# Performance work log

Measured on AMD Instinct MI355X. Metric: run time of the kernel, lower is better.

Reference implementation:

```python
import jax, jax.numpy as jnp
import numpy as np

P, R, S = 512, 128, 128   # num_proposal, ref_length, src_length
K = 3                      # top-k per row/column
THRESHOLD = 0.05
MUTUAL = False
CONDITIONAL = True


def setup_inputs() -> dict:
    key = jax.random.key(0)
    k1, k2, k3, k4 = jax.random.split(key, 4)
    return {
        "matching_score_map": jax.random.normal(k1, (P, R, S), dtype=jnp.float32),
        "ref_knn_masks": jax.random.bernoulli(k2, 0.9, (P, R)),
        "src_knn_masks": jax.random.bernoulli(k3, 0.9, (P, S)),
        "node_corr_scores": jax.random.uniform(k4, (P,), dtype=jnp.float32),
    }


def reference(matching_score_map, ref_knn_masks, src_knn_masks, node_corr_scores):
    # matching_score_map: [P, R, S] log-scores -> exp, as in torch forward
    m = jnp.exp(matching_score_map)
    p, r, s = m.shape
    # corr_mask_map = ref_mask[:, :, None] & src_mask[:, None, :] -> [P, R, S]
    corr_mask_map = jnp.logical_and(ref_knn_masks[:, :, None], src_knn_masks[:, None, :])

    pidx = jnp.arange(p)[:, None, None]

    # top-k along src dim (dim=2), scatter back into a sparse score map
    ref_topk_scores, ref_topk_idx = jax.lax.top_k(m, K)           # [P, R, K]
    ridx = jnp.arange(r)[None, :, None]
    ref_score_map = jnp.zeros_like(m).at[pidx, ridx, ref_topk_idx].set(ref_topk_scores)

    # top-k along ref dim (dim=1): transpose, top_k, scatter, transpose back
    mt = jnp.swapaxes(m, 1, 2)                                    # [P, S, R]
    src_topk_scores, src_topk_idx = jax.lax.top_k(mt, K)          # [P, S, K]
    sidx = jnp.arange(s)[None, :, None]
    src_score_map = jnp.swapaxes(
        jnp.zeros_like(mt).at[pidx, sidx, src_topk_idx].set(src_topk_scores), 1, 2
    )

    ref_corr_map = jnp.logical_and(ref_score_map > THRESHOLD, corr_mask_map)
    src_corr_map = jnp.logical_and(src_score_map > THRESHOLD, corr_mask_map)

    score_map = (ref_score_map + src_score_map) * 0.5
    if MUTUAL:
        corr_map = jnp.logical_and(ref_corr_map, src_corr_map)
    else:
        corr_map = jnp.logical_or(ref_corr_map, src_corr_map)
    if CONDITIONAL:
        score_map = score_map * node_corr_scores[:, None, None]
    return score_map, corr_map
```

## Files before the change

### kernel.cpp

```cpp
#include <hip/hip_runtime.h>


constexpr int NP = 512;
constexpr int NR = 128;
constexpr int NS = 128;
constexpr int RS = NR * NS;
constexpr float THRESHOLD = 0.05f;
constexpr float NEG_INF = -3.4e38f;

__device__ __forceinline__ void top3_insert(float v, float& m0, float& m1, float& m2) {
    bool g2 = v > m2, g1 = v > m1, g0 = v > m0;
    float n2 = g1 ? m1 : (g2 ? v : m2);
    float n1 = g0 ? m0 : (g1 ? v : m1);
    float n0 = g0 ? v : m0;
    m0 = n0; m1 = n1; m2 = n2;
}

__device__ __forceinline__ float third_of_merge(float a0, float a1, float a2,
                                                float b0, float b1, float b2) {
    float third = NEG_INF;
    #pragma unroll
    for (int k = 0; k < 3; ++k) {
        bool ta = a0 >= b0;
        third = ta ? a0 : b0;
        float na0 = ta ? a1 : a0, na1 = ta ? a2 : a1;
        float nb0 = ta ? b0 : b1, nb1 = ta ? b1 : b2;
        a0 = na0; a1 = na1; a2 = ta ? NEG_INF : a2;
        b0 = nb0; b1 = nb1; b2 = ta ? b2 : NEG_INF;
    }
    return third;
}

__global__ __launch_bounds__(256) void thresholds_kernel(
    const float* __restrict__ in, float* __restrict__ ws)
{
    const int b = blockIdx.x;
    const int p = b >> 1;
    const int t = threadIdx.x;
    const float* base = in + (size_t)p * RS;
    __shared__ float mbuf[NS * 3];

    if (b & 1) {
        const int row = t >> 1, half = t & 1;
        const float4* r4 = (const float4*)(base + row * NS + half * 64);
        float m0 = NEG_INF, m1 = NEG_INF, m2 = NEG_INF;
        #pragma unroll
        for (int k = 0; k < 16; ++k) {
            float4 v = r4[k];
            top3_insert(v.x, m0, m1, m2);
            top3_insert(v.y, m0, m1, m2);
            top3_insert(v.z, m0, m1, m2);
            top3_insert(v.w, m0, m1, m2);
        }
        float o0 = __shfl_xor(m0, 1);
        float o1 = __shfl_xor(m1, 1);
        float o2 = __shfl_xor(m2, 1);
        float third = third_of_merge(m0, m1, m2, o0, o1, o2);
        if (half == 0) ws[p * 256 + 128 + row] = third;
    } else {
        const int col = t & 127, rh = t >> 7;
        const float* c0 = base + (size_t)(rh * 64) * NS + col;
        float m0 = NEG_INF, m1 = NEG_INF, m2 = NEG_INF;
        #pragma unroll 16
        for (int r = 0; r < 64; ++r)
            top3_insert(c0[r * NS], m0, m1, m2);
        if (rh) {
            mbuf[col * 3 + 0] = m0; mbuf[col * 3 + 1] = m1; mbuf[col * 3 + 2] = m2;
        }
        __syncthreads();
        if (!rh) {
            float third = third_of_merge(m0, m1, m2,
                                         mbuf[col * 3], mbuf[col * 3 + 1], mbuf[col * 3 + 2]);
            ws[p * 256 + col] = third;
        }
    }
}

__global__ __launch_bounds__(256) void epilogue_kernel(
    const float* __restrict__ in,
    const int*   __restrict__ rmask,
    const int*   __restrict__ smask,
    const float* __restrict__ ncs,
    const float* __restrict__ ws,
    float*       __restrict__ out)
{
    const int gid = blockIdx.x * 256 + threadIdx.x;
    const int p   = gid >> 12;
    const int rem = gid & 4095;
    const int r   = rem >> 5;
    const int c4  = rem & 31;

    const float4 x   = ((const float4*)in)[gid];
    const float  tr  = ws[p * 256 + 128 + r];
    const float4 tc  = ((const float4*)(ws + p * 256))[c4];
    const bool   mr  = rmask[p * NR + r] != 0;
    const int4   ms  = ((const int4*)(smask + (size_t)p * NS))[c4];
    const float  nc  = ncs[p];

    float4 sc, co;
    {   float m  = __expf(x.x);
        float rs = (x.x >= tr)   ? m : 0.f;
        float cs = (x.x >= tc.x) ? m : 0.f;
        sc.x = 0.5f * (rs + cs) * nc;
        co.x = (mr && (ms.x != 0) && (rs > THRESHOLD || cs > THRESHOLD)) ? 1.f : 0.f; }
    {   float m  = __expf(x.y);
        float rs = (x.y >= tr)   ? m : 0.f;
        float cs = (x.y >= tc.y) ? m : 0.f;
        sc.y = 0.5f * (rs + cs) * nc;
        co.y = (mr && (ms.y != 0) && (rs > THRESHOLD || cs > THRESHOLD)) ? 1.f : 0.f; }
    {   float m  = __expf(x.z);
        float rs = (x.z >= tr)   ? m : 0.f;
        float cs = (x.z >= tc.z) ? m : 0.f;
        sc.z = 0.5f * (rs + cs) * nc;
        co.z = (mr && (ms.z != 0) && (rs > THRESHOLD || cs > THRESHOLD)) ? 1.f : 0.f; }
    {   float m  = __expf(x.w);
        float rs = (x.w >= tr)   ? m : 0.f;
        float cs = (x.w >= tc.w) ? m : 0.f;
        sc.w = 0.5f * (rs + cs) * nc;
        co.w = (mr && (ms.w != 0) && (rs > THRESHOLD || cs > THRESHOLD)) ? 1.f : 0.f; }

    ((float4*)out)[gid] = sc;
    ((float4*)(out + (size_t)NP * RS))[gid] = co;
}

extern "C" void kernel_launch(void* const* d_in, const int* in_sizes, int n_in,
                              void* d_out, int out_size, void* d_ws, size_t ws_size,
                              hipStream_t stream) {
    const float* msm   = (const float*)d_in[0];
    const int*   rmask = (const int*)  d_in[1];
    const int*   smask = (const int*)  d_in[2];
    const float* ncs   = (const float*)d_in[3];
    float* out = (float*)d_out;
    float* ws  = (float*)d_ws;

    thresholds_kernel<<<2 * NP, 256, 0, stream>>>(msm, ws);
    epilogue_kernel<<<NP * RS / 4 / 256, 256, 0, stream>>>(msm, rmask, smask, ncs, ws, out);
}
```

Measured before the change: 110.1 us.

## Fuse top-k threshold and epilogue kernels via per-proposal LDS tile

Replaces the two-kernel design with one kernel that runs one 512-thread block per proposal. Each block stages the whole 128x128 score tile in LDS, computes the row and column third-largest thresholds with shuffle-based top-3 merges, then applies the exp/threshold/mask epilogue from LDS. This removes the second global read of the input and one kernel launch. In exchange, 64KB of LDS per block limits blocks per CU, and with only 512 blocks there is little overlap between the load, compute and store phases; the column pass may also hit LDS bank conflicts.

```diff
diff --git a/kernel.cpp b/kernel.cpp
--- a/kernel.cpp
+++ b/kernel.cpp
@@ -16,111 +16,120 @@
     m0 = n0; m1 = n1; m2 = n2;
 }
 
-__device__ __forceinline__ float third_of_merge(float a0, float a1, float a2,
-                                                float b0, float b1, float b2) {
-    float third = NEG_INF;
-    #pragma unroll
-    for (int k = 0; k < 3; ++k) {
-        bool ta = a0 >= b0;
-        third = ta ? a0 : b0;
-        float na0 = ta ? a1 : a0, na1 = ta ? a2 : a1;
-        float nb0 = ta ? b0 : b1, nb1 = ta ? b1 : b2;
-        a0 = na0; a1 = na1; a2 = ta ? NEG_INF : a2;
-        b0 = nb0; b1 = nb1; b2 = ta ? b2 : NEG_INF;
-    }
-    return third;
+__device__ __forceinline__ void shfl_merge3(int d, float& m0, float& m1, float& m2) {
+    float o0 = __shfl_xor(m0, d);
+    float o1 = __shfl_xor(m1, d);
+    float o2 = __shfl_xor(m2, d);
+    top3_insert(o0, m0, m1, m2);
+    top3_insert(o1, m0, m1, m2);
+    top3_insert(o2, m0, m1, m2);
 }
 
-__global__ __launch_bounds__(256) void thresholds_kernel(
-    const float* __restrict__ in, float* __restrict__ ws)
+__global__ __launch_bounds__(512, 4) void fused_kernel(
+    const float* __restrict__ in,
+    const int*   __restrict__ rmask,
+    const int*   __restrict__ smask,
+    const float* __restrict__ ncs,
+    float*       __restrict__ ws,
+    float*       __restrict__ out)
 {
-    const int b = blockIdx.x;
-    const int p = b >> 1;
+    __shared__ float tile[RS];
+    const int p = blockIdx.x;
     const int t = threadIdx.x;
-    const float* base = in + (size_t)p * RS;
-    __shared__ float mbuf[NS * 3];
 
-    if (b & 1) {
-        const int row = t >> 1, half = t & 1;
-        const float4* r4 = (const float4*)(base + row * NS + half * 64);
+    const float4* b4 = (const float4*)(in + (size_t)p * RS);
+    float4*       t4 = (float4*)tile;
+
+    #pragma unroll
+    for (int k = 0; k < 8; ++k) {
+        int i4 = t + k * 512;
+        t4[i4] = b4[i4];
+    }
+    __syncthreads();
+
+    float* ws_row = ws + (size_t)p * 256;
+    float* ws_col = ws_row + 128;
+
+    {
+        const int row = t >> 2, q = t & 3;
+        const int base4 = row * 32 + q * 8;
         float m0 = NEG_INF, m1 = NEG_INF, m2 = NEG_INF;
         #pragma unroll
-        for (int k = 0; k < 16; ++k) {
-            float4 v = r4[k];
+        for (int j = 0; j < 8; ++j) {
+            int jj = (j + t) & 7;
+            float4 v = t4[base4 + jj];
             top3_insert(v.x, m0, m1, m2);
             top3_insert(v.y, m0, m1, m2);
             top3_insert(v.z, m0, m1, m2);
             top3_insert(v.w, m0, m1, m2);
         }
-        float o0 = __shfl_xor(m0, 1);
-        float o1 = __shfl_xor(m1, 1);
-        float o2 = __shfl_xor(m2, 1);
-        float third = third_of_merge(m0, m1, m2, o0, o1, o2);
-        if (half == 0) ws[p * 256 + 128 + row] = third;
-    } else {
-        const int col = t & 127, rh = t >> 7;
-        const float* c0 = base + (size_t)(rh * 64) * NS + col;
+        shfl_merge3(1, m0, m1, m2);
+        shfl_merge3(2, m0, m1, m2);
+        if (q == 0) ws_row[row] = m2;
+    }
+
+    {
+        const int col = t >> 2, seg = t & 3;
         float m0 = NEG_INF, m1 = NEG_INF, m2 = NEG_INF;
-        #pragma unroll 16
-        for (int r = 0; r < 64; ++r)
-            top3_insert(c0[r * NS], m0, m1, m2);
-        if (rh) {
-            mbuf[col * 3 + 0] = m0; mbuf[col * 3 + 1] = m1; mbuf[col * 3 + 2] = m2;
+        #pragma unroll 8
+        for (int i = 0; i < 32; ++i) {
+            float v = tile[(seg * 32 + i) * NS + col];
+            top3_insert(v, m0, m1, m2);
         }
-        __syncthreads();
-        if (!rh) {
-            float third = third_of_merge(m0, m1, m2,
-                                         mbuf[col * 3], mbuf[col * 3 + 1], mbuf[col * 3 + 2]);
-            ws[p * 256 + col] = third;
-        }
+        shfl_merge3(1, m0, m1, m2);
+        shfl_merge3(2, m0, m1, m2);
+        if (seg == 0) ws_col[col] = m2;
     }
-}
 
-__global__ __launch_bounds__(256) void epilogue_kernel(
-    const float* __restrict__ in,
-    const int*   __restrict__ rmask,
-    const int*   __restrict__ smask,
-    const float* __restrict__ ncs,
-    const float* __restrict__ ws,
-    float*       __restrict__ out)
-{
-    const int gid = blockIdx.x * 256 + threadIdx.x;
-    const int p   = gid >> 12;
-    const int rem = gid & 4095;
-    const int r   = rem >> 5;
-    const int c4  = rem & 31;
+    __threadfence_block();
+    __syncthreads();
 
-    const float4 x   = ((const float4*)in)[gid];
-    const float  tr  = ws[p * 256 + 128 + r];
-    const float4 tc  = ((const float4*)(ws + p * 256))[c4];
-    const bool   mr  = rmask[p * NR + r] != 0;
-    const int4   ms  = ((const int4*)(smask + (size_t)p * NS))[c4];
-    const float  nc  = ncs[p];
+    const float  nc = ncs[p];
+    const float4 tc = ((const float4*)ws_col)[t & 31];
+    const int4   ms = ((const int4*)(smask + (size_t)p * NS))[t & 31];
+    float trow[8];
+    int   mrow[8];
+    #pragma unroll
+    for (int k = 0; k < 8; ++k) {
+        int row = (t >> 5) + k * 16;
+        trow[k] = ws_row[row];
+        mrow[k] = rmask[p * NR + row];
+    }
 
-    float4 sc, co;
-    {   float m  = __expf(x.x);
-        float rs = (x.x >= tr)   ? m : 0.f;
-        float cs = (x.x >= tc.x) ? m : 0.f;
-        sc.x = 0.5f * (rs + cs) * nc;
-        co.x = (mr && (ms.x != 0) && (rs > THRESHOLD || cs > THRESHOLD)) ? 1.f : 0.f; }
-    {   float m  = __expf(x.y);
-        float rs = (x.y >= tr)   ? m : 0.f;
-        float cs = (x.y >= tc.y) ? m : 0.f;
-        sc.y = 0.5f * (rs + cs) * nc;
-        co.y = (mr && (ms.y != 0) && (rs > THRESHOLD || cs > THRESHOLD)) ? 1.f : 0.f; }
-    {   float m  = __expf(x.z);
-        float rs = (x.z >= tr)   ? m : 0.f;
-        float cs = (x.z >= tc.z) ? m : 0.f;
-        sc.z = 0.5f * (rs + cs) * nc;
-        co.z = (mr && (ms.z != 0) && (rs > THRESHOLD || cs > THRESHOLD)) ? 1.f : 0.f; }
-    {   float m  = __expf(x.w);
-        float rs = (x.w >= tr)   ? m : 0.f;
-        float cs = (x.w >= tc.w) ? m : 0.f;
-        sc.w = 0.5f * (rs + cs) * nc;
-        co.w = (mr && (ms.w != 0) && (rs > THRESHOLD || cs > THRESHOLD)) ? 1.f : 0.f; }
+    float4* sc4 = (float4*)(out + (size_t)p * RS);
+    float4* co4 = (float4*)(out + (size_t)(NP + p) * RS);
+    #pragma unroll
+    for (int k = 0; k < 8; ++k) {
+        int C = t + k * 512;
+        float4 x = t4[C];
+        float tr = trow[k];
+        bool  mr = mrow[k] != 0;
+        float4 sc, co;
 
-    ((float4*)out)[gid] = sc;
-    ((float4*)(out + (size_t)NP * RS))[gid] = co;
+        {   float m  = __expf(x.x);
+            float rs = (x.x >= tr)   ? m : 0.f;
+            float cs = (x.x >= tc.x) ? m : 0.f;
+            sc.x = 0.5f * (rs + cs) * nc;
+            co.x = (mr && (ms.x != 0) && (rs > THRESHOLD || cs > THRESHOLD)) ? 1.f : 0.f; }
+        {   float m  = __expf(x.y);
+            float rs = (x.y >= tr)   ? m : 0.f;
+            float cs = (x.y >= tc.y) ? m : 0.f;
+            sc.y = 0.5f * (rs + cs) * nc;
+            co.y = (mr && (ms.y != 0) && (rs > THRESHOLD || cs > THRESHOLD)) ? 1.f : 0.f; }
+        {   float m  = __expf(x.z);
+            float rs = (x.z >= tr)   ? m : 0.f;
+            float cs = (x.z >= tc.z) ? m : 0.f;
+            sc.z = 0.5f * (rs + cs) * nc;
+            co.z = (mr && (ms.z != 0) && (rs > THRESHOLD || cs > THRESHOLD)) ? 1.f : 0.f; }
+        {   float m  = __expf(x.w);
+            float rs = (x.w >= tr)   ? m : 0.f;
+            float cs = (x.w >= tc.w) ? m : 0.f;
+            sc.w = 0.5f * (rs + cs) * nc;
+            co.w = (mr && (ms.w != 0) && (rs > THRESHOLD || cs > THRESHOLD)) ? 1.f : 0.f; }
+
+        sc4[C] = sc;
+        co4[C] = co;
+    }
 }
 
 extern "C" void kernel_launch(void* const* d_in, const int* in_sizes, int n_in,
@@ -133,6 +142,5 @@
     float* out = (float*)d_out;
     float* ws  = (float*)d_ws;
 
-    thresholds_kernel<<<2 * NP, 256, 0, stream>>>(msm, ws);
-    epilogue_kernel<<<NP * RS / 4 / 256, 256, 0, stream>>>(msm, rmask, smask, ncs, ws, out);
+    fused_kernel<<<NP, 512, 0, stream>>>(msm, rmask, smask, ncs, ws, out);
 }
```

Result: faster. 98.16 us (-10.8%).
